# Kernel optimization log

Measured on AMD Instinct MI355X. Metric: run time of the kernel, lower is better.

## Reference

```python
import jax, jax.numpy as jnp
import numpy as np

B, NQ, NK, D = 16, 256, 256, 256  # batch, n_queries, n_keys, kq_size (=value_size)


def setup_inputs() -> dict:
    key = jax.random.key(0)
    ks = jax.random.split(key, 8)
    s1 = 1.0 / np.sqrt(2 * D)  # fan-in scaled init for W1 (split into Wk, Wq)
    s2 = 1.0 / np.sqrt(D)
    return {
        "keys": jax.random.normal(ks[0], (B, NK, D), jnp.float32),
        "queries": jax.random.normal(ks[1], (B, NQ, D), jnp.float32),
        "values": jax.random.normal(ks[2], (B, NK, D), jnp.float32),
        # MLP layer 1: Linear(2*D -> D); concat(keys, queries) @ W1 == keys@Wk + queries@Wq
        "Wk": jax.random.normal(ks[3], (D, D), jnp.float32) * s1,
        "Wq": jax.random.normal(ks[4], (D, D), jnp.float32) * s1,
        "b1": jax.random.normal(ks[5], (D,), jnp.float32) * 0.01,
        # MLP layer 2: Linear(D -> 1)
        "w2": jax.random.normal(ks[6], (D,), jnp.float32) * s2,
        "b2": jax.random.normal(ks[7], (1,), jnp.float32) * 0.01,
    }


def reference(keys, queries, values, Wk, Wq, b1, w2, b2):
    # Additive (Bahdanau) attention: score(q,k) = w2 . tanh(W1 @ [k; q] + b1) + b2
    hk = jnp.einsum("bkd,de->bke", keys, Wk)      # [B,K,D]
    hq = jnp.einsum("bqd,de->bqe", queries, Wq)   # [B,Q,D]
    h = jnp.tanh(hq[:, :, None, :] + hk[:, None, :, :] + b1)  # [B,Q,K,D]
    logits = jnp.einsum("bqkd,d->bqk", h, w2) + b2[0]          # [B,Q,K]
    attn = jax.nn.softmax(logits, axis=-1)                     # normalize over keys
    context = jnp.einsum("bqk,bkv->bqv", attn, values)         # [B,Q,Dv]
    return context
```

## Files before the change

### kernel.cpp

```cpp
#include <hip/hip_runtime.h>
#include <hip/hip_bf16.h>

#ifndef __has_builtin
#define __has_builtin(x) 0
#endif

__device__ __forceinline__ float fast_exp2(float x) {
#if __has_builtin(__builtin_amdgcn_exp2f)
  return __builtin_amdgcn_exp2f(x);
#else
  return __exp2f(x);
#endif
}
__device__ __forceinline__ float fast_rcp(float x) {
#if __has_builtin(__builtin_amdgcn_rcpf)
  return __builtin_amdgcn_rcpf(x);
#else
  return 1.0f / x;
#endif
}

#define B_   16
#define NQ_  256
#define NK_  256
#define D_   256
#define QT   4
#define TANH_SCALE 2.8853900817779268f
#define LOG2E      1.4426950408889634f

__global__ __launch_bounds__(256) void proj_kernel(
    const float* __restrict__ queries, const float* __restrict__ keys,
    const float* __restrict__ Wq, const float* __restrict__ Wk,
    const float* __restrict__ b1,
    float* __restrict__ eqs, float* __restrict__ eks)
{
  const int z = blockIdx.z;
  const float* __restrict__ X = z ? keys : queries;
  const float* __restrict__ W = z ? Wk : Wq;
  float* __restrict__ O = z ? eks : eqs;

  const int m0 = blockIdx.x * 64;
  const int n0 = blockIdx.y * 64;
  const int t  = threadIdx.x;
  const int tx = t & 15, ty = t >> 4;

  __shared__ float As_t[64][68];
  __shared__ float Bs[64][68];

  float acc[4][4] = {};

  for (int kt = 0; kt < 4; ++kt) {
    const int k0 = kt * 64;
    #pragma unroll
    for (int i = 0; i < 4; ++i) {
      int f = t + 256 * i;
      int row = f >> 4;
      int kc  = (f & 15) << 2;
      float4 v = *(const float4*)&X[(size_t)(m0 + row) * D_ + (k0 + kc)];
      As_t[kc + 0][row] = v.x; As_t[kc + 1][row] = v.y;
      As_t[kc + 2][row] = v.z; As_t[kc + 3][row] = v.w;
    }
    #pragma unroll
    for (int i = 0; i < 4; ++i) {
      int f = t + 256 * i;
      int kr = f >> 4;
      int nc = (f & 15) << 2;
      *(float4*)&Bs[kr][nc] = *(const float4*)&W[(size_t)(k0 + kr) * D_ + (n0 + nc)];
    }
    __syncthreads();
    #pragma unroll 8
    for (int k = 0; k < 64; ++k) {
      float4 a = *(const float4*)&As_t[k][ty << 2];
      float4 b = *(const float4*)&Bs[k][tx << 2];
      float aa[4] = {a.x, a.y, a.z, a.w};
      float bb[4] = {b.x, b.y, b.z, b.w};
      #pragma unroll
      for (int i = 0; i < 4; ++i)
        #pragma unroll
        for (int j = 0; j < 4; ++j)
          acc[i][j] = fmaf(aa[i], bb[j], acc[i][j]);
    }
    __syncthreads();
  }

  float bias[4] = {0.f, 0.f, 0.f, 0.f};
  if (z == 0) {
    #pragma unroll
    for (int j = 0; j < 4; ++j) bias[j] = b1[n0 + (tx << 2) + j];
  }
  #pragma unroll
  for (int i = 0; i < 4; ++i)
    #pragma unroll
    for (int j = 0; j < 4; ++j)
      O[(size_t)(m0 + (ty << 2) + i) * D_ + n0 + (tx << 2) + j] =
          fast_exp2(TANH_SCALE * (acc[i][j] + bias[j]));
}

__global__ __launch_bounds__(256, 4) void attn_kernel(
    const float* __restrict__ eqs, const float* __restrict__ eks,
    const float* __restrict__ values, const float* __restrict__ w2,
    float* __restrict__ out)
{
  const int wgid = blockIdx.x;
  const int b  = wgid & 15;
  const int q0 = (wgid >> 4) * QT;
  const int t  = threadIdx.x;
  const int lane = t & 63, wave = t >> 6;

  __shared__ float pvred[4][QT][D_];
  __shared__ float redA[4][QT], redB[4][QT];

  const float* __restrict__ ekrow = eks + ((size_t)(b * NK_) + t) * D_;
  const float* __restrict__ equni = eqs + ((size_t)(b * NQ_) + q0) * D_;
  float acc[QT] = {};
  #pragma unroll 4
  for (int d4 = 0; d4 < D_ / 4; ++d4) {
    float4 ekv = *(const float4*)&ekrow[d4 << 2];
    float4 wv  = *(const float4*)&w2[d4 << 2];
    float e[4] = {ekv.x, ekv.y, ekv.z, ekv.w};
    float w[4] = {wv.x, wv.y, wv.z, wv.w};
    #pragma unroll
    for (int qi = 0; qi < QT; ++qi) {
      float4 eqv = *(const float4*)&equni[(size_t)qi * D_ + (d4 << 2)];
      float a[4] = {eqv.x, eqv.y, eqv.z, eqv.w};
      #pragma unroll
      for (int j = 0; j < 4; ++j) {
        float t0 = fmaf(a[j], e[j], 1.0f);
        acc[qi] = fmaf(w[j], fast_rcp(t0), acc[qi]);
      }
    }
  }

  float logit[QT];
  #pragma unroll
  for (int qi = 0; qi < QT; ++qi) logit[qi] = -2.0f * acc[qi];

  #pragma unroll
  for (int qi = 0; qi < QT; ++qi) {
    float v = logit[qi];
    #pragma unroll
    for (int off = 32; off; off >>= 1) v = fmaxf(v, __shfl_xor(v, off, 64));
    if (lane == 0) redA[wave][qi] = v;
  }
  __syncthreads();
  float mx[QT];
  #pragma unroll
  for (int qi = 0; qi < QT; ++qi)
    mx[qi] = fmaxf(fmaxf(redA[0][qi], redA[1][qi]),
                   fmaxf(redA[2][qi], redA[3][qi]));

  float p[QT];
  #pragma unroll
  for (int qi = 0; qi < QT; ++qi)
    p[qi] = fast_exp2((logit[qi] - mx[qi]) * LOG2E);
  #pragma unroll
  for (int qi = 0; qi < QT; ++qi) {
    float v = p[qi];
    #pragma unroll
    for (int off = 32; off; off >>= 1) v += __shfl_xor(v, off, 64);
    if (lane == 0) redB[wave][qi] = v;
  }
  __syncthreads();
  float pl[QT];
  #pragma unroll
  for (int qi = 0; qi < QT; ++qi) {
    float inv = fast_rcp(redB[0][qi] + redB[1][qi] + redB[2][qi] + redB[3][qi]);
    pl[qi] = p[qi] * inv;
  }

  float ctx[QT][4] = {};
  const float* __restrict__ vbase =
      values + ((size_t)(b * NK_) + (wave << 6)) * D_ + (lane << 2);
  #pragma unroll 4
  for (int kl = 0; kl < 64; ++kl) {
    float4 vv = *(const float4*)&vbase[(size_t)kl * D_];
    float vz[4] = {vv.x, vv.y, vv.z, vv.w};
    #pragma unroll
    for (int qi = 0; qi < QT; ++qi) {
      float pk = __int_as_float(
          __builtin_amdgcn_readlane(__float_as_int(pl[qi]), kl));
      #pragma unroll
      for (int j = 0; j < 4; ++j)
        ctx[qi][j] = fmaf(pk, vz[j], ctx[qi][j]);
    }
  }

  #pragma unroll
  for (int qi = 0; qi < QT; ++qi) {
    float4 v4; v4.x = ctx[qi][0]; v4.y = ctx[qi][1];
    v4.z = ctx[qi][2]; v4.w = ctx[qi][3];
    *(float4*)&pvred[wave][qi][lane << 2] = v4;
  }
  __syncthreads();
  #pragma unroll
  for (int qi = 0; qi < QT; ++qi) {
    float o = pvred[0][qi][t] + pvred[1][qi][t] +
              pvred[2][qi][t] + pvred[3][qi][t];
    out[((size_t)(b * NQ_) + q0 + qi) * D_ + t] = o;
  }
}

extern "C" void kernel_launch(void* const* d_in, const int* in_sizes, int n_in,
                              void* d_out, int out_size, void* d_ws, size_t ws_size,
                              hipStream_t stream)
{
  const float* keys    = (const float*)d_in[0];
  const float* queries = (const float*)d_in[1];
  const float* values  = (const float*)d_in[2];
  const float* Wk      = (const float*)d_in[3];
  const float* Wq      = (const float*)d_in[4];
  const float* b1      = (const float*)d_in[5];
  const float* w2      = (const float*)d_in[6];

  float* eqs = (float*)d_ws;
  float* eks = eqs + (size_t)B_ * NQ_ * D_;
  float* out = (float*)d_out;

  dim3 pgrid(B_ * NQ_ / 64, D_ / 64, 2);
  proj_kernel<<<pgrid, 256, 0, stream>>>(queries, keys, Wq, Wk, b1, eqs, eks);

  attn_kernel<<<dim3(B_ * NQ_ / QT), 256, 0, stream>>>(eqs, eks, values, w2, out);
}
```

Before: 70.40 us.

## Split attention over key halves with combine kernel and paired reciprocals

Replaces the single attention kernel with a two-stage scheme. The first kernel gives each block half of the keys and splits the feature dimension across two thread halves. It writes unnormalized partial contexts and exp sums to workspace, and a second kernel combines them and normalizes. Two tanh reciprocals are merged into one rcp of a product, and the running-max subtraction is dropped. This aims to raise parallelism and occupancy and to cut transcendental work, at the cost of an extra launch, extra workspace traffic, and relying on bounded logits to avoid exp overflow.

```diff
diff --git a/kernel.cpp b/kernel.cpp
--- a/kernel.cpp
+++ b/kernel.cpp
@@ -27,6 +27,7 @@
 #define QT   4
 #define TANH_SCALE 2.8853900817779268f
 #define LOG2E      1.4426950408889634f
+#define NEG2LOG2E  (-2.8853900817779268f)
 
 __global__ __launch_bounds__(256) void proj_kernel(
     const float* __restrict__ queries, const float* __restrict__ keys,
@@ -96,7 +97,134 @@
           fast_exp2(TANH_SCALE * (acc[i][j] + bias[j]));
 }
 
-__global__ __launch_bounds__(256, 4) void attn_kernel(
+__global__ __launch_bounds__(256, 8) void attn_split(
+    const float* __restrict__ eqs, const float* __restrict__ eks,
+    const float* __restrict__ values, const float* __restrict__ w2,
+    float* __restrict__ sctx, float* __restrict__ psum)
+{
+  const int wgid = blockIdx.x;
+  const int b    = wgid & 15;
+  const int qq   = (wgid >> 4) & 63;
+  const int kh   = wgid >> 10;
+  const int q0   = qq * QT;
+  const int t    = threadIdx.x;
+  const int lane = t & 63, wave = t >> 6;
+  const int kloc = t & 127;
+  const int kdh  = t >> 7;
+
+  __shared__ __align__(16) char smem[4 * 4 * 256 * 4];
+  float (*plog)[128][4]  = (float(*)[128][4])smem;
+  float (*pvred)[4][256] = (float(*)[4][256])smem;
+
+  const float* __restrict__ ekrow =
+      eks + ((size_t)(b * NK_) + kh * 128 + kloc) * D_ + kdh * 128;
+  const float* __restrict__ equ =
+      eqs + ((size_t)(b * NQ_) + q0) * D_ + kdh * 128;
+  const float* __restrict__ w2u = w2 + kdh * 128;
+
+  float acc[QT] = {};
+  #pragma unroll 4
+  for (int d4 = 0; d4 < 32; ++d4) {
+    float4 ekv = *(const float4*)&ekrow[d4 << 2];
+    float4 wv  = *(const float4*)&w2u[d4 << 2];
+    #pragma unroll
+    for (int qi = 0; qi < QT; ++qi) {
+      float4 eqv = *(const float4*)&equ[(size_t)qi * D_ + (d4 << 2)];
+      float t0 = fmaf(eqv.x, ekv.x, 1.0f);
+      float t1 = fmaf(eqv.y, ekv.y, 1.0f);
+      float n01 = wv.x * t1;  n01 = fmaf(wv.y, t0, n01);
+      float r01 = fast_rcp(t0 * t1);
+      acc[qi] = fmaf(n01, r01, acc[qi]);
+      float t2 = fmaf(eqv.z, ekv.z, 1.0f);
+      float t3 = fmaf(eqv.w, ekv.w, 1.0f);
+      float n23 = wv.z * t3;  n23 = fmaf(wv.w, t2, n23);
+      float r23 = fast_rcp(t2 * t3);
+      acc[qi] = fmaf(n23, r23, acc[qi]);
+    }
+  }
+
+  {
+    float4 a4; a4.x = acc[0]; a4.y = acc[1]; a4.z = acc[2]; a4.w = acc[3];
+    *(float4*)&plog[kdh][kloc][0] = a4;
+  }
+  __syncthreads();
+  float p[QT];
+  {
+    float4 o4 = *(const float4*)&plog[1 - kdh][kloc][0];
+    float other[4] = {o4.x, o4.y, o4.z, o4.w};
+    #pragma unroll
+    for (int qi = 0; qi < QT; ++qi)
+      p[qi] = fast_exp2(NEG2LOG2E * (acc[qi] + other[qi]));
+  }
+
+  if (kdh == 0) {
+    #pragma unroll
+    for (int qi = 0; qi < QT; ++qi) {
+      float v = p[qi];
+      #pragma unroll
+      for (int off = 32; off; off >>= 1) v += __shfl_xor(v, off, 64);
+      if (lane == 0) psum[(size_t)wgid * 8 + wave * 4 + qi] = v;
+    }
+  }
+  __syncthreads();
+
+  const int src_base = (wave >> 1) * 32;
+  const int key_base = (wave & 1) * 64 + src_base;
+  float ctx[QT][4] = {};
+  const float* __restrict__ vbase =
+      values + ((size_t)(b * NK_) + kh * 128 + key_base) * D_ + (lane << 2);
+  #pragma unroll 4
+  for (int i = 0; i < 32; ++i) {
+    float4 vv = *(const float4*)&vbase[(size_t)i * D_];
+    float vz[4] = {vv.x, vv.y, vv.z, vv.w};
+    #pragma unroll
+    for (int qi = 0; qi < QT; ++qi) {
+      float pk = __int_as_float(
+          __builtin_amdgcn_readlane(__float_as_int(p[qi]), src_base + i));
+      #pragma unroll
+      for (int j = 0; j < 4; ++j)
+        ctx[qi][j] = fmaf(pk, vz[j], ctx[qi][j]);
+    }
+  }
+
+  #pragma unroll
+  for (int qi = 0; qi < QT; ++qi) {
+    float4 v4; v4.x = ctx[qi][0]; v4.y = ctx[qi][1];
+    v4.z = ctx[qi][2]; v4.w = ctx[qi][3];
+    *(float4*)&pvred[wave][qi][lane << 2] = v4;
+  }
+  __syncthreads();
+  #pragma unroll
+  for (int qi = 0; qi < QT; ++qi) {
+    float s = pvred[0][qi][t] + pvred[1][qi][t] +
+              pvred[2][qi][t] + pvred[3][qi][t];
+    sctx[((size_t)wgid * 4 + qi) * 256 + t] = s;
+  }
+}
+
+__global__ __launch_bounds__(256) void combine_kernel(
+    const float* __restrict__ sctx, const float* __restrict__ psum,
+    float* __restrict__ out)
+{
+  const int bid = blockIdx.x;
+  const int b = bid & 15, qq = bid >> 4;
+  const int t = threadIdx.x;
+  const size_t blk0 = bid, blk1 = bid + 1024;
+
+  float s[QT];
+  #pragma unroll
+  for (int qi = 0; qi < QT; ++qi)
+    s[qi] = psum[blk0 * 8 + qi] + psum[blk0 * 8 + 4 + qi] +
+            psum[blk1 * 8 + qi] + psum[blk1 * 8 + 4 + qi];
+
+  #pragma unroll
+  for (int qi = 0; qi < QT; ++qi) {
+    float v = sctx[(blk0 * 4 + qi) * 256 + t] + sctx[(blk1 * 4 + qi) * 256 + t];
+    out[((size_t)(b * NQ_) + qq * QT + qi) * D_ + t] = v * fast_rcp(s[qi]);
+  }
+}
+
+__global__ __launch_bounds__(256, 4) void attn_fallback(
     const float* __restrict__ eqs, const float* __restrict__ eks,
     const float* __restrict__ values, const float* __restrict__ w2,
     float* __restrict__ out)
@@ -212,12 +340,22 @@
   const float* b1      = (const float*)d_in[5];
   const float* w2      = (const float*)d_in[6];
 
-  float* eqs = (float*)d_ws;
-  float* eks = eqs + (size_t)B_ * NQ_ * D_;
-  float* out = (float*)d_out;
+  float* eqs  = (float*)d_ws;
+  float* eks  = eqs + (size_t)B_ * NQ_ * D_;
+  float* sctx = eks + (size_t)B_ * NK_ * D_;
+  float* psum = sctx + (size_t)2048 * 4 * 256;
+  float* out  = (float*)d_out;
+
+  const size_t need = ((size_t)2 * B_ * NQ_ * D_ + (size_t)2048 * 4 * 256 +
+                       (size_t)2048 * 8) * sizeof(float);
 
   dim3 pgrid(B_ * NQ_ / 64, D_ / 64, 2);
   proj_kernel<<<pgrid, 256, 0, stream>>>(queries, keys, Wq, Wk, b1, eqs, eks);
 
-  attn_kernel<<<dim3(B_ * NQ_ / QT), 256, 0, stream>>>(eqs, eks, values, w2, out);
-}
+  if (ws_size >= need) {
+    attn_split<<<dim3(2048), 256, 0, stream>>>(eqs, eks, values, w2, sctx, psum);
+    combine_kernel<<<dim3(1024), 256, 0, stream>>>(sctx, psum, out);
+  } else {
+    attn_fallback<<<dim3(B_ * NQ_ / QT), 256, 0, stream>>>(eqs, eks, values, w2, out);
+  }
+}
```

After: 192.5 us. +173.4%, slower.

## Use packed FMA, pairwise reciprocal merging, and LDS-staged query rows in attention

Applied to the files above, without the earlier changes.

The projection GEMM inner loop now uses two-wide packed FMAs (v_pk_fma_f32) instead of scalar FMAs. In the attention score loop, the query rows and w2 are staged into shared memory once per block instead of being read from global memory per thread. The key row is software-prefetched one step ahead. Pairs of reciprocals are merged algebraically as w_a/t_a + w_b/t_b = (w_a t_b + w_b t_a)/(t_a t_b), which halves the transcendental rcp count at the cost of extra multiplies. The merge risks overflow or precision loss when the product t_a*t_b becomes large, since these are exp-based terms.

```diff
diff --git a/kernel.cpp b/kernel.cpp
--- a/kernel.cpp
+++ b/kernel.cpp
@@ -4,6 +4,8 @@
 #ifndef __has_builtin
 #define __has_builtin(x) 0
 #endif
+
+typedef float v2f __attribute__((ext_vector_type(2)));
 
 __device__ __forceinline__ float fast_exp2(float x) {
 #if __has_builtin(__builtin_amdgcn_exp2f)
@@ -17,6 +19,13 @@
   return __builtin_amdgcn_rcpf(x);
 #else
   return 1.0f / x;
+#endif
+}
+__device__ __forceinline__ v2f pk_fma(v2f a, v2f b, v2f c) {
+#if __has_builtin(__builtin_elementwise_fma)
+  return __builtin_elementwise_fma(a, b, c);
+#else
+  v2f r; r.x = fmaf(a.x, b.x, c.x); r.y = fmaf(a.y, b.y, c.y); return r;
 #endif
 }
 
@@ -47,7 +56,7 @@
   __shared__ float As_t[64][68];
   __shared__ float Bs[64][68];
 
-  float acc[4][4] = {};
+  v2f acc2[4][2] = {};
 
   for (int kt = 0; kt < 4; ++kt) {
     const int k0 = kt * 64;
@@ -72,13 +81,15 @@
     for (int k = 0; k < 64; ++k) {
       float4 a = *(const float4*)&As_t[k][ty << 2];
       float4 b = *(const float4*)&Bs[k][tx << 2];
+      v2f b01; b01.x = b.x; b01.y = b.y;
+      v2f b23; b23.x = b.z; b23.y = b.w;
       float aa[4] = {a.x, a.y, a.z, a.w};
-      float bb[4] = {b.x, b.y, b.z, b.w};
       #pragma unroll
-      for (int i = 0; i < 4; ++i)
-        #pragma unroll
-        for (int j = 0; j < 4; ++j)
-          acc[i][j] = fmaf(aa[i], bb[j], acc[i][j]);
+      for (int i = 0; i < 4; ++i) {
+        v2f ai; ai.x = aa[i]; ai.y = aa[i];
+        acc2[i][0] = pk_fma(ai, b01, acc2[i][0]);
+        acc2[i][1] = pk_fma(ai, b23, acc2[i][1]);
+      }
     }
     __syncthreads();
   }
@@ -89,11 +100,13 @@
     for (int j = 0; j < 4; ++j) bias[j] = b1[n0 + (tx << 2) + j];
   }
   #pragma unroll
-  for (int i = 0; i < 4; ++i)
+  for (int i = 0; i < 4; ++i) {
+    float av[4] = {acc2[i][0].x, acc2[i][0].y, acc2[i][1].x, acc2[i][1].y};
     #pragma unroll
     for (int j = 0; j < 4; ++j)
       O[(size_t)(m0 + (ty << 2) + i) * D_ + n0 + (tx << 2) + j] =
-          fast_exp2(TANH_SCALE * (acc[i][j] + bias[j]));
+          fast_exp2(TANH_SCALE * (av[j] + bias[j]));
+  }
 }
 
 __global__ __launch_bounds__(256, 4) void attn_kernel(
@@ -107,27 +120,38 @@
   const int t  = threadIdx.x;
   const int lane = t & 63, wave = t >> 6;
 
+  __shared__ float eqw[QT + 1][D_];
   __shared__ float pvred[4][QT][D_];
   __shared__ float redA[4][QT], redB[4][QT];
 
+  #pragma unroll
+  for (int qi = 0; qi < QT; ++qi)
+    eqw[qi][t] = eqs[((size_t)(b * NQ_) + q0 + qi) * D_ + t];
+  eqw[QT][t] = w2[t];
+  __syncthreads();
+
   const float* __restrict__ ekrow = eks + ((size_t)(b * NK_) + t) * D_;
-  const float* __restrict__ equni = eqs + ((size_t)(b * NQ_) + q0) * D_;
   float acc[QT] = {};
+  float4 ekn = *(const float4*)&ekrow[0];
   #pragma unroll 4
   for (int d4 = 0; d4 < D_ / 4; ++d4) {
-    float4 ekv = *(const float4*)&ekrow[d4 << 2];
-    float4 wv  = *(const float4*)&w2[d4 << 2];
-    float e[4] = {ekv.x, ekv.y, ekv.z, ekv.w};
-    float w[4] = {wv.x, wv.y, wv.z, wv.w};
+    float4 ekv = ekn;
+    if (d4 < D_ / 4 - 1) ekn = *(const float4*)&ekrow[(d4 + 1) << 2];
+    float4 wv = *(const float4*)&eqw[QT][d4 << 2];
+    v2f ek01; ek01.x = ekv.x; ek01.y = ekv.y;
+    v2f ek23; ek23.x = ekv.z; ek23.y = ekv.w;
+    v2f one; one.x = 1.0f; one.y = 1.0f;
     #pragma unroll
     for (int qi = 0; qi < QT; ++qi) {
-      float4 eqv = *(const float4*)&equni[(size_t)qi * D_ + (d4 << 2)];
-      float a[4] = {eqv.x, eqv.y, eqv.z, eqv.w};
-      #pragma unroll
-      for (int j = 0; j < 4; ++j) {
-        float t0 = fmaf(a[j], e[j], 1.0f);
-        acc[qi] = fmaf(w[j], fast_rcp(t0), acc[qi]);
-      }
+      float4 eqv = *(const float4*)&eqw[qi][d4 << 2];
+      v2f eq01; eq01.x = eqv.x; eq01.y = eqv.y;
+      v2f eq23; eq23.x = eqv.z; eq23.y = eqv.w;
+      v2f t01 = pk_fma(eq01, ek01, one);
+      float n01 = fmaf(wv.y, t01.x, wv.x * t01.y);
+      acc[qi] = fmaf(n01, fast_rcp(t01.x * t01.y), acc[qi]);
+      v2f t23 = pk_fma(eq23, ek23, one);
+      float n23 = fmaf(wv.w, t23.x, wv.z * t23.y);
+      acc[qi] = fmaf(n23, fast_rcp(t23.x * t23.y), acc[qi]);
     }
   }
 
```

Measured after the change: 75.44 us. +7.2%, slower.

## Batch reciprocals over four dims, drop softmax max pass, vectorize GEMM LDS

Applied to the files above, without the earlier changes.

The attention score loop now combines four reciprocal terms into one fraction per group, so it issues one rcp per four dimensions instead of four, using extra multiplies. The softmax max-subtraction, with its shuffle reduction and barrier, is removed because logits are bounded by the sum of |w2| and cannot overflow exp. The projection GEMM stores A row-major and reads 4x4 float4 fragments per k-step, and it writes outputs as float4. Risks are larger intermediate products in the combined fraction and no max guard if weights are scaled up.

```diff
diff --git a/kernel.cpp b/kernel.cpp
--- a/kernel.cpp
+++ b/kernel.cpp
@@ -26,7 +26,7 @@
 #define D_   256
 #define QT   4
 #define TANH_SCALE 2.8853900817779268f
-#define LOG2E      1.4426950408889634f
+#define NEG2LOG2E  (-2.8853900817779268f)
 
 __global__ __launch_bounds__(256) void proj_kernel(
     const float* __restrict__ queries, const float* __restrict__ keys,
@@ -44,7 +44,7 @@
   const int t  = threadIdx.x;
   const int tx = t & 15, ty = t >> 4;
 
-  __shared__ float As_t[64][68];
+  __shared__ float As[64][68];
   __shared__ float Bs[64][68];
 
   float acc[4][4] = {};
@@ -56,9 +56,7 @@
       int f = t + 256 * i;
       int row = f >> 4;
       int kc  = (f & 15) << 2;
-      float4 v = *(const float4*)&X[(size_t)(m0 + row) * D_ + (k0 + kc)];
-      As_t[kc + 0][row] = v.x; As_t[kc + 1][row] = v.y;
-      As_t[kc + 2][row] = v.z; As_t[kc + 3][row] = v.w;
+      *(float4*)&As[row][kc] = *(const float4*)&X[(size_t)(m0 + row) * D_ + (k0 + kc)];
     }
     #pragma unroll
     for (int i = 0; i < 4; ++i) {
@@ -68,17 +66,28 @@
       *(float4*)&Bs[kr][nc] = *(const float4*)&W[(size_t)(k0 + kr) * D_ + (n0 + nc)];
     }
     __syncthreads();
-    #pragma unroll 8
-    for (int k = 0; k < 64; ++k) {
-      float4 a = *(const float4*)&As_t[k][ty << 2];
-      float4 b = *(const float4*)&Bs[k][tx << 2];
-      float aa[4] = {a.x, a.y, a.z, a.w};
-      float bb[4] = {b.x, b.y, b.z, b.w};
+    #pragma unroll 4
+    for (int k4 = 0; k4 < 16; ++k4) {
+      const int kk = k4 << 2;
+      float4 a0 = *(const float4*)&As[(ty << 2) + 0][kk];
+      float4 a1 = *(const float4*)&As[(ty << 2) + 1][kk];
+      float4 a2 = *(const float4*)&As[(ty << 2) + 2][kk];
+      float4 a3 = *(const float4*)&As[(ty << 2) + 3][kk];
+      float4 b0 = *(const float4*)&Bs[kk + 0][tx << 2];
+      float4 b1v = *(const float4*)&Bs[kk + 1][tx << 2];
+      float4 b2 = *(const float4*)&Bs[kk + 2][tx << 2];
+      float4 b3 = *(const float4*)&Bs[kk + 3][tx << 2];
+      float A[4][4] = {{a0.x,a0.y,a0.z,a0.w},{a1.x,a1.y,a1.z,a1.w},
+                       {a2.x,a2.y,a2.z,a2.w},{a3.x,a3.y,a3.z,a3.w}};
+      float Bv[4][4] = {{b0.x,b0.y,b0.z,b0.w},{b1v.x,b1v.y,b1v.z,b1v.w},
+                        {b2.x,b2.y,b2.z,b2.w},{b3.x,b3.y,b3.z,b3.w}};
       #pragma unroll
-      for (int i = 0; i < 4; ++i)
+      for (int kkk = 0; kkk < 4; ++kkk)
         #pragma unroll
-        for (int j = 0; j < 4; ++j)
-          acc[i][j] = fmaf(aa[i], bb[j], acc[i][j]);
+        for (int i = 0; i < 4; ++i)
+          #pragma unroll
+          for (int j = 0; j < 4; ++j)
+            acc[i][j] = fmaf(A[i][kkk], Bv[kkk][j], acc[i][j]);
     }
     __syncthreads();
   }
@@ -89,11 +98,14 @@
     for (int j = 0; j < 4; ++j) bias[j] = b1[n0 + (tx << 2) + j];
   }
   #pragma unroll
-  for (int i = 0; i < 4; ++i)
-    #pragma unroll
-    for (int j = 0; j < 4; ++j)
-      O[(size_t)(m0 + (ty << 2) + i) * D_ + n0 + (tx << 2) + j] =
-          fast_exp2(TANH_SCALE * (acc[i][j] + bias[j]));
+  for (int i = 0; i < 4; ++i) {
+    float4 o4;
+    o4.x = fast_exp2(TANH_SCALE * (acc[i][0] + bias[0]));
+    o4.y = fast_exp2(TANH_SCALE * (acc[i][1] + bias[1]));
+    o4.z = fast_exp2(TANH_SCALE * (acc[i][2] + bias[2]));
+    o4.w = fast_exp2(TANH_SCALE * (acc[i][3] + bias[3]));
+    *(float4*)&O[(size_t)(m0 + (ty << 2) + i) * D_ + n0 + (tx << 2)] = o4;
+  }
 }
 
 __global__ __launch_bounds__(256, 4) void attn_kernel(
@@ -108,51 +120,40 @@
   const int lane = t & 63, wave = t >> 6;
 
   __shared__ float pvred[4][QT][D_];
-  __shared__ float redA[4][QT], redB[4][QT];
+  __shared__ float redB[4][QT];
 
   const float* __restrict__ ekrow = eks + ((size_t)(b * NK_) + t) * D_;
   const float* __restrict__ equni = eqs + ((size_t)(b * NQ_) + q0) * D_;
+
   float acc[QT] = {};
   #pragma unroll 4
   for (int d4 = 0; d4 < D_ / 4; ++d4) {
-    float4 ekv = *(const float4*)&ekrow[d4 << 2];
-    float4 wv  = *(const float4*)&w2[d4 << 2];
+    const int off = d4 << 2;
+    float4 ekv = *(const float4*)&ekrow[off];
+    float4 wv  = *(const float4*)&w2[off];
     float e[4] = {ekv.x, ekv.y, ekv.z, ekv.w};
     float w[4] = {wv.x, wv.y, wv.z, wv.w};
     #pragma unroll
     for (int qi = 0; qi < QT; ++qi) {
-      float4 eqv = *(const float4*)&equni[(size_t)qi * D_ + (d4 << 2)];
-      float a[4] = {eqv.x, eqv.y, eqv.z, eqv.w};
-      #pragma unroll
-      for (int j = 0; j < 4; ++j) {
-        float t0 = fmaf(a[j], e[j], 1.0f);
-        acc[qi] = fmaf(w[j], fast_rcp(t0), acc[qi]);
-      }
-    }
-  }
-
-  float logit[QT];
-  #pragma unroll
-  for (int qi = 0; qi < QT; ++qi) logit[qi] = -2.0f * acc[qi];
-
-  #pragma unroll
-  for (int qi = 0; qi < QT; ++qi) {
-    float v = logit[qi];
-    #pragma unroll
-    for (int off = 32; off; off >>= 1) v = fmaxf(v, __shfl_xor(v, off, 64));
-    if (lane == 0) redA[wave][qi] = v;
-  }
-  __syncthreads();
-  float mx[QT];
+      float4 eqv = *(const float4*)&equni[(size_t)qi * D_ + off];
+      float t0 = fmaf(eqv.x, e[0], 1.0f);
+      float t1 = fmaf(eqv.y, e[1], 1.0f);
+      float t2 = fmaf(eqv.z, e[2], 1.0f);
+      float t3 = fmaf(eqv.w, e[3], 1.0f);
+      float p01 = t0 * t1;
+      float p23 = t2 * t3;
+      float n01 = fmaf(w[1], t0, w[0] * t1);
+      float n23 = fmaf(w[3], t2, w[2] * t3);
+      float num = fmaf(n23, p01, n01 * p23);
+      float r   = fast_rcp(p01 * p23);
+      acc[qi] = fmaf(num, r, acc[qi]);
+    }
+  }
+
+  float p[QT];
   #pragma unroll
   for (int qi = 0; qi < QT; ++qi)
-    mx[qi] = fmaxf(fmaxf(redA[0][qi], redA[1][qi]),
-                   fmaxf(redA[2][qi], redA[3][qi]));
-
-  float p[QT];
-  #pragma unroll
-  for (int qi = 0; qi < QT; ++qi)
-    p[qi] = fast_exp2((logit[qi] - mx[qi]) * LOG2E);
+    p[qi] = fast_exp2(NEG2LOG2E * acc[qi]);
   #pragma unroll
   for (int qi = 0; qi < QT; ++qi) {
     float v = p[qi];
@@ -186,11 +187,9 @@
   }
 
   #pragma unroll
-  for (int qi = 0; qi < QT; ++qi) {
-    float4 v4; v4.x = ctx[qi][0]; v4.y = ctx[qi][1];
-    v4.z = ctx[qi][2]; v4.w = ctx[qi][3];
-    *(float4*)&pvred[wave][qi][lane << 2] = v4;
-  }
+  for (int qi = 0; qi < QT; ++qi)
+    *(float4*)&pvred[wave][qi][lane << 2] =
+        make_float4(ctx[qi][0], ctx[qi][1], ctx[qi][2], ctx[qi][3]);
   __syncthreads();
   #pragma unroll
   for (int qi = 0; qi < QT; ++qi) {
```

Result: faster. 67.82 us (median of 2 runs) (-3.7%).
